# Optimization experiments

Measured on AMD Instinct MI355X. Metric: run time of the kernel, lower is better.

## Reference

```python
import jax, jax.numpy as jnp
import numpy as np

B, N, C, H = 2, 2048, 1024, 16
D = C // H  # head dim = 64
SCALE = 1.0 / np.sqrt(D)
BASE = 10000.0  # ntk_factor=1.0 => base unchanged


def setup_inputs() -> dict:
    key = jax.random.key(0)
    k1, k2, k3, k4 = jax.random.split(key, 4)
    x = jax.random.normal(k1, (B, N, C), dtype=jnp.float32)
    Wqkv = jax.random.normal(k2, (C, 3 * C), dtype=jnp.float32) * (1.0 / np.sqrt(C))
    Wout = jax.random.normal(k3, (C, C), dtype=jnp.float32) * (1.0 / np.sqrt(C))
    bout = jax.random.normal(k4, (C,), dtype=jnp.float32) * 0.01
    return {"x": x, "Wqkv": Wqkv, "Wout": Wout, "bout": bout}


def _rope_tables(n, d, dtype):
    inv_freq = 1.0 / (BASE ** (jnp.arange(0, d, 2, dtype=jnp.float32) / d))
    t = jnp.arange(n, dtype=jnp.float32)
    freqs = t[:, None] * inv_freq[None, :]            # [N, D/2]
    cos = jnp.cos(freqs)[None, :, None, :].astype(dtype)  # [1,N,1,D/2]
    sin = jnp.sin(freqs)[None, :, None, :].astype(dtype)
    return cos, sin


def _apply_rope(u, cos, sin):
    # u: [B,N,H,D]; strided-halves RoPE variant (cat, not interleave)
    u1, u2 = u[..., ::2], u[..., 1::2]
    return jnp.concatenate([u1 * cos - u2 * sin, u1 * sin + u2 * cos], axis=-1)


def reference(x, Wqkv, Wout, bout):
    b, n, c = x.shape
    qkv = (x @ Wqkv).reshape(b, n, 3, H, D)
    q, k, v = qkv[:, :, 0], qkv[:, :, 1], qkv[:, :, 2]  # [B,N,H,D]
    cos, sin = _rope_tables(n, D, x.dtype)
    q = _apply_rope(q, cos, sin)
    k = _apply_rope(k, cos, sin)
    scores = jnp.einsum("bqhd,bkhd->bhqk", q, k) * SCALE
    causal = jnp.triu(jnp.ones((n, n), dtype=bool), k=1)
    scores = jnp.where(causal, -jnp.inf, scores)
    attn = jax.nn.softmax(scores, axis=-1)
    out = jnp.einsum("bhqk,bkhd->bqhd", attn, v).reshape(b, n, c)
    return out @ Wout + bout
```

## Files before the change

### kernel.cpp

```cpp
#include <hip/hip_runtime.h>
#include <hip/hip_bf16.h>
#include <math.h>

#define B_ 2
#define N_ 2048
#define C_ 1024
#define H_ 16
#define D_ 64
#define M_ 4096
#define QKV_N 3072
#define SCALE_ 0.125f
#define FIXM 8.0f
#define L2E 1.442695041f

typedef unsigned short u16;
typedef unsigned int u32;
using bf16x8   = __attribute__((ext_vector_type(8))) __bf16;
using ushortx8 = __attribute__((ext_vector_type(8))) unsigned short;
using floatx4  = __attribute__((ext_vector_type(4))) float;

__device__ __forceinline__ float bf2f(u16 u) {
    union { u32 i; float f; } v; v.i = ((u32)u) << 16; return v.f;
}
__device__ __forceinline__ u16 f2bf(float f) {
    union { float f; u32 i; } v; v.f = f;
    u32 r = (v.i + 0x7fff + ((v.i >> 16) & 1)) >> 16;
    return (u16)r;
}
__device__ __forceinline__ u32 pk2bf(float a, float b) {
    __hip_bfloat162 h = __float22bfloat162_rn(make_float2(a, b));
    union { __hip_bfloat162 h; u32 u; } c; c.h = h; return c.u;
}

__device__ __forceinline__ void gl2lds16(const void* g, void* l) {
    __builtin_amdgcn_global_load_lds(
        (const __attribute__((address_space(1))) unsigned int*)(unsigned long long)g,
        (__attribute__((address_space(3))) unsigned int*)(unsigned long long)l,
        16, 0, 0);
}

__constant__ unsigned char UQI[24] = {7,15,15,14,14,6,13,13,12,12,5,11,11,10,10,4,9,9,8,8,3,2,1,0};
__constant__ unsigned char UT0[24] = {0,0,16,0,15,0,0,14,0,13,0,0,12,0,11,0,0,10,0,9,0,0,0,0};
__constant__ unsigned char UNT[24] = {16,16,16,15,15,14,14,14,13,13,12,12,12,11,11,10,10,10,9,9,8,6,4,2};

__device__ __forceinline__ void do_convtrans(const float* W, u16* Wt, int K, int N,
                                             int nb, int kb, int tid) {
    int n = nb * 256 + tid;
    int k0 = kb * 128;
    #pragma unroll
    for (int kk = 0; kk < 128; kk += 8) {
        ushortx8 v;
        #pragma unroll
        for (int j = 0; j < 8; j++)
            v[j] = f2bf(W[(size_t)(k0 + kk + j) * N + n]);
        *(ushortx8*)(&Wt[(size_t)n * K + k0 + kk]) = v;
    }
}

__global__ __launch_bounds__(256) void prep_kernel(
    const float* __restrict__ x, const float* __restrict__ Wqkv,
    float* __restrict__ cosT, float* __restrict__ sinT,
    u16* __restrict__ xb, u16* __restrict__ Wqkvt)
{
    int bid = blockIdx.x, tid = threadIdx.x;
    if (bid < 2048) {
        int i = bid * 256 + tid;
        const float4* p = (const float4*)x + (size_t)i * 2;
        float4 a = p[0], b = p[1];
        ushortx8 v;
        v[0] = f2bf(a.x); v[1] = f2bf(a.y); v[2] = f2bf(a.z); v[3] = f2bf(a.w);
        v[4] = f2bf(b.x); v[5] = f2bf(b.y); v[6] = f2bf(b.z); v[7] = f2bf(b.w);
        *(ushortx8*)(xb + (size_t)i * 8) = v;
    } else if (bid < 2304) {
        int idx = (bid - 2048) * 256 + tid;
        int n = idx >> 5, i = idx & 31;
        double inv = pow(10000.0, -(double)i / 32.0);
        double f = (double)n * inv;
        cosT[idx] = (float)cos(f);
        sinT[idx] = (float)sin(f);
    } else {
        int u = bid - 2304;
        do_convtrans(Wqkv, Wqkvt, C_, QKV_N, u % 12, u / 12, tid);
    }
}

__global__ __launch_bounds__(256) void gemm128(
    const u16* __restrict__ A, const u16* __restrict__ Bt,
    void* __restrict__ Cm, const float* __restrict__ bias, int fp32out,
    int M, int N, int K)
{
    __shared__ u16 As[128 * 32];
    __shared__ u16 Bs[128 * 32];
    const int t = threadIdx.x;
    const int w = t >> 6, lane = t & 63;
    const int quad = lane >> 4, cc = lane & 15;
    const int m0 = blockIdx.y * 128, n0 = blockIdx.x * 128;
    const int wm = (w >> 1) * 64, wn = (w & 1) * 64;

    floatx4 acc[4][4];
    floatx4 zero = {0.f, 0.f, 0.f, 0.f};
    #pragma unroll
    for (int i = 0; i < 4; i++)
        #pragma unroll
        for (int j = 0; j < 4; j++) acc[i][j] = zero;

    const int srow = lane >> 2, skof = (lane & 3) * 8;

    for (int k0 = 0; k0 < K; k0 += 32) {
        __syncthreads();
        #pragma unroll
        for (int c = 0; c < 2; c++) {
            int chunk = w * 2 + c;
            int row = chunk * 16 + srow;
            gl2lds16(A  + (size_t)(m0 + row) * K + k0 + skof, (char*)As + chunk * 1024);
            gl2lds16(Bt + (size_t)(n0 + row) * K + k0 + skof, (char*)Bs + chunk * 1024);
        }
        __syncthreads();

        bf16x8 af[4], bf[4];
        #pragma unroll
        for (int i = 0; i < 4; i++)
            af[i] = *(const bf16x8*)(&As[(wm + i * 16 + cc) * 32 + quad * 8]);
        #pragma unroll
        for (int j = 0; j < 4; j++)
            bf[j] = *(const bf16x8*)(&Bs[(wn + j * 16 + cc) * 32 + quad * 8]);
        #pragma unroll
        for (int i = 0; i < 4; i++)
            #pragma unroll
            for (int j = 0; j < 4; j++)
                acc[i][j] = __builtin_amdgcn_mfma_f32_16x16x32_bf16(af[i], bf[j], acc[i][j], 0, 0, 0);
    }

    #pragma unroll
    for (int i = 0; i < 4; i++)
        #pragma unroll
        for (int j = 0; j < 4; j++)
            #pragma unroll
            for (int r = 0; r < 4; r++) {
                int row = m0 + wm + i * 16 + quad * 4 + r;
                int col = n0 + wn + j * 16 + cc;
                float v = acc[i][j][r];
                if (fp32out) ((float*)Cm)[(size_t)row * N + col] = v + bias[col];
                else         ((u16*)Cm)[(size_t)row * N + col] = f2bf(v);
            }
}

__global__ void rope_kernel(const u16* __restrict__ qkv,
                            const float* __restrict__ cosT, const float* __restrict__ sinT,
                            u16* __restrict__ Qh, u16* __restrict__ Kh, u16* __restrict__ Vh)
{
    int idx = blockIdx.x * 256 + threadIdx.x;
    if (idx >= B_ * N_ * H_ * 32) return;
    int i = idx & 31;
    int h = (idx >> 5) & (H_ - 1);
    int n = (idx >> 9) & (N_ - 1);
    int b = idx >> 20;
    size_t m = (size_t)b * N_ + n;
    const u16* row = qkv + m * QKV_N;
    float cs = cosT[n * 32 + i], sn = sinT[n * 32 + i];

    float q1 = bf2f(row[h * 64 + 2 * i]),      q2 = bf2f(row[h * 64 + 2 * i + 1]);
    float k1 = bf2f(row[C_ + h * 64 + 2 * i]), k2 = bf2f(row[C_ + h * 64 + 2 * i + 1]);
    size_t obase = ((size_t)(b * H_ + h) * N_ + n) * D_;
    Qh[obase + i]      = f2bf((q1 * cs - q2 * sn) * SCALE_);
    Qh[obase + 32 + i] = f2bf((q1 * sn + q2 * cs) * SCALE_);
    Kh[obase + i]      = f2bf(k1 * cs - k2 * sn);
    Kh[obase + 32 + i] = f2bf(k1 * sn + k2 * cs);
    Vh[obase + 2 * i]     = row[2 * C_ + h * 64 + 2 * i];
    Vh[obase + 2 * i + 1] = row[2 * C_ + h * 64 + 2 * i + 1];
}

__global__ __launch_bounds__(256) void attn_kernel(
    const u16* __restrict__ Qh, const u16* __restrict__ Kh,
    const u16* __restrict__ Vh, u16* __restrict__ Ao,
    u16* __restrict__ Opart, float* __restrict__ lpart)
{
    constexpr int LDK = 66;
    __shared__ u16 Ks[2][64 * LDK];
    __shared__ u16 Vs[2][64 * LDK];
    __shared__ u16 Ps[4 * 32 * LDK];

    const int t = threadIdx.x;
    const int wave = t >> 6, lane = t & 63;
    const int quad = lane >> 4, cc = lane & 15;
    const int u = blockIdx.x;
    const int qi = UQI[u], tile0 = UT0[u], ntl = UNT[u];
    const int qb0 = qi * 128;
    const int bh = blockIdx.y;
    const size_t hb = (size_t)bh * N_ * D_;

    bf16x8 qf[2][2];
    #pragma unroll
    for (int qt = 0; qt < 2; qt++) {
        const u16* qrow = Qh + hb + (size_t)(qb0 + qt * 64 + wave * 16 + cc) * D_;
        qf[qt][0] = *(const bf16x8*)(qrow + quad * 8);
        qf[qt][1] = *(const bf16x8*)(qrow + 32 + quad * 8);
    }

    floatx4 zero = {0.f, 0.f, 0.f, 0.f};
    floatx4 Oacc[2][4];
    float lsum[2] = {0.f, 0.f};
    #pragma unroll
    for (int qt = 0; qt < 2; qt++)
        #pragma unroll
        for (int j = 0; j < 4; j++) Oacc[qt][j] = zero;

    const int krow = t >> 3, kch = (t & 7) * 8;
    const int kp = t >> 3, vchunk = (t & 7) * 8;
    const int qlocal = wave * 16 + cc;
    u32* psd = (u32*)Ps;

    bf16x8 kr[2]; ushortx8 vr[2];
    {
        int kb = tile0 * 64;
        kr[0] = *(const bf16x8*)(Kh + hb + (size_t)(kb + krow) * D_ + kch);
        kr[1] = *(const bf16x8*)(Kh + hb + (size_t)(kb + krow + 32) * D_ + kch);
        vr[0] = *(const ushortx8*)(Vh + hb + (size_t)(kb + 2 * kp) * D_ + vchunk);
        vr[1] = *(const ushortx8*)(Vh + hb + (size_t)(kb + 2 * kp + 1) * D_ + vchunk);
    }

    for (int ti = 0; ti < ntl; ti++) {
        const int kb = (tile0 + ti) * 64;
        const int c = ti & 1;
        *(bf16x8*)(&Ks[c][krow * LDK + kch]) = kr[0];
        *(bf16x8*)(&Ks[c][(krow + 32) * LDK + kch]) = kr[1];
        u32* vsd = (u32*)Vs[c];
        #pragma unroll
        for (int e = 0; e < 8; e++)
            vsd[(vchunk + e) * 33 + kp] = (u32)vr[0][e] | ((u32)vr[1][e] << 16);
        if (ti + 1 < ntl) {
            int kb2 = (tile0 + ti + 1) * 64;
            kr[0] = *(const bf16x8*)(Kh + hb + (size_t)(kb2 + krow) * D_ + kch);
            kr[1] = *(const bf16x8*)(Kh + hb + (size_t)(kb2 + krow + 32) * D_ + kch);
            vr[0] = *(const ushortx8*)(Vh + hb + (size_t)(kb2 + 2 * kp) * D_ + vchunk);
            vr[1] = *(const ushortx8*)(Vh + hb + (size_t)(kb2 + 2 * kp + 1) * D_ + vchunk);
        }
        __syncthreads();

        const bool act0 = (kb <= qb0);

        floatx4 S[2][4];
        #pragma unroll
        for (int nt = 0; nt < 4; nt++) {
            bf16x8 kf0 = *(const bf16x8*)(&Ks[c][(nt * 16 + cc) * LDK + quad * 8]);
            bf16x8 kf1 = *(const bf16x8*)(&Ks[c][(nt * 16 + cc) * LDK + 32 + quad * 8]);
            floatx4 a1 = zero;
            a1 = __builtin_amdgcn_mfma_f32_16x16x32_bf16(kf0, qf[1][0], a1, 0, 0, 0);
            a1 = __builtin_amdgcn_mfma_f32_16x16x32_bf16(kf1, qf[1][1], a1, 0, 0, 0);
            S[1][nt] = a1;
            if (act0) {
                floatx4 a0 = zero;
                a0 = __builtin_amdgcn_mfma_f32_16x16x32_bf16(kf0, qf[0][0], a0, 0, 0, 0);
                a0 = __builtin_amdgcn_mfma_f32_16x16x32_bf16(kf1, qf[0][1], a0, 0, 0, 0);
                S[0][nt] = a0;
            }
        }

        #pragma unroll
        for (int qt = 0; qt < 2; qt++) {
            if (qt == 0 && !act0) continue;
            const bool diag = (kb == qb0 + qt * 64);
            const int prow = (wave * 32 + qt * 16 + cc) * 33;
            #pragma unroll
            for (int nt = 0; nt < 4; nt++) {
                float p[4];
                #pragma unroll
                for (int r = 0; r < 4; r++) {
                    int key_l = nt * 16 + quad * 4 + r;
                    float e = exp2f(fmaf(S[qt][nt][r], L2E, -FIXM * L2E));
                    p[r] = (diag && (key_l > qlocal)) ? 0.0f : e;
                    lsum[qt] += p[r];
                }
                psd[prow + nt * 8 + quad * 2]     = pk2bf(p[0], p[1]);
                psd[prow + nt * 8 + quad * 2 + 1] = pk2bf(p[2], p[3]);
            }
        }

        #pragma unroll
        for (int s = 0; s < 2; s++) {
            bf16x8 pf1 = *(const bf16x8*)(&Ps[(wave * 32 + 16 + cc) * LDK + s * 32 + quad * 8]);
            bf16x8 pf0;
            if (act0) pf0 = *(const bf16x8*)(&Ps[(wave * 32 + cc) * LDK + s * 32 + quad * 8]);
            #pragma unroll
            for (int j = 0; j < 4; j++) {
                bf16x8 vf = *(const bf16x8*)(&Vs[c][(j * 16 + cc) * LDK + s * 32 + quad * 8]);
                Oacc[1][j] = __builtin_amdgcn_mfma_f32_16x16x32_bf16(pf1, vf, Oacc[1][j], 0, 0, 0);
                if (act0)
                    Oacc[0][j] = __builtin_amdgcn_mfma_f32_16x16x32_bf16(pf0, vf, Oacc[0][j], 0, 0, 0);
            }
        }
    }

    const bool partial = (qi >= 8);
    const int cid = (tile0 > 0) ? 1 : 0;
    const int slot = ((bh * 8 + (qi - 8)) * 2 + cid);
    const int b = bh >> 4, h = bh & (H_ - 1);

    #pragma unroll
    for (int qt = 0; qt < 2; qt++) {
        float lf = lsum[qt];
        lf += __shfl_xor(lf, 16, 64);
        lf += __shfl_xor(lf, 32, 64);
        if (!partial) {
            #pragma unroll
            for (int r = 0; r < 4; r++) {
                float l_r = __shfl(lf, quad * 4 + r, 64);
                float inv = 1.0f / l_r;
                int n = qb0 + qt * 64 + wave * 16 + quad * 4 + r;
                #pragma unroll
                for (int j = 0; j < 4; j++)
                    Ao[((size_t)b * N_ + n) * C_ + h * D_ + j * 16 + cc] = f2bf(Oacc[qt][j][r] * inv);
            }
        } else {
            #pragma unroll
            for (int r = 0; r < 4; r++) {
                int lrow = qt * 64 + wave * 16 + quad * 4 + r;
                u16* Ob = Opart + (size_t)slot * (128 * 64) + (size_t)lrow * 64;
                #pragma unroll
                for (int j = 0; j < 4; j++)
                    Ob[j * 16 + cc] = f2bf(Oacc[qt][j][r]);
            }
            if (lane < 16)
                lpart[slot * 128 + qt * 64 + wave * 16 + cc] = lf;
        }
    }
}

__global__ __launch_bounds__(256) void attn_combine(
    const u16* __restrict__ Opart, const float* __restrict__ lpart,
    u16* __restrict__ Ao, const float* __restrict__ Wout, u16* __restrict__ Woutt)
{
    if (blockIdx.x >= 2048) {
        int u = blockIdx.x - 2048;
        do_convtrans(Wout, Woutt, C_, C_, u % 4, u / 4, threadIdx.x);
        return;
    }
    int g = blockIdx.x * 256 + threadIdx.x;
    int f4 = g & 15;
    int row = (g >> 4) & 127;
    int qz = (g >> 11) & 7;
    int bh = g >> 14;
    int s0 = (bh * 8 + qz) * 2;
    const u16* O0 = Opart + (size_t)s0 * (128 * 64) + (size_t)row * 64 + f4 * 4;
    const u16* O1 = O0 + 128 * 64;
    float l = lpart[s0 * 128 + row] + lpart[(s0 + 1) * 128 + row];
    float inv = 1.0f / l;
    ushort4 a = *(const ushort4*)O0, c = *(const ushort4*)O1;
    int b = bh >> 4, h = bh & (H_ - 1);
    int n = (qz + 8) * 128 + row;
    u16* d = Ao + ((size_t)b * N_ + n) * C_ + h * D_ + f4 * 4;
    d[0] = f2bf((bf2f(a.x) + bf2f(c.x)) * inv);
    d[1] = f2bf((bf2f(a.y) + bf2f(c.y)) * inv);
    d[2] = f2bf((bf2f(a.z) + bf2f(c.z)) * inv);
    d[3] = f2bf((bf2f(a.w) + bf2f(c.w)) * inv);
}

extern "C" void kernel_launch(void* const* d_in, const int* in_sizes, int n_in,
                              void* d_out, int out_size, void* d_ws, size_t ws_size,
                              hipStream_t stream)
{
    const float* x    = (const float*)d_in[0];
    const float* Wqkv = (const float*)d_in[1];
    const float* Wout = (const float*)d_in[2];
    const float* bout = (const float*)d_in[3];

    char* p = (char*)d_ws;
    u16* qkv = (u16*)p; p += (size_t)M_ * QKV_N * 2;
    u16* Qh  = (u16*)p; p += (size_t)B_ * H_ * N_ * D_ * 2;
    u16* Kh  = (u16*)p; p += (size_t)B_ * H_ * N_ * D_ * 2;
    u16* Vh  = (u16*)p; p += (size_t)B_ * H_ * N_ * D_ * 2;
    u16* Ao  = (u16*)p; p += (size_t)M_ * C_ * 2;
    float* cosT = (float*)p; p += (size_t)N_ * 32 * 4;
    float* sinT = (float*)p; p += (size_t)N_ * 32 * 4;

    u16* xb    = Ao;
    u16* Wqkvt = Qh;
    u16* Woutt = qkv;
    u16* Opart = (u16*)((char*)qkv + ((size_t)2 << 20));
    float* lpart = (float*)((char*)qkv + ((size_t)21 << 20));

    hipLaunchKernelGGL(prep_kernel, dim3(2400), dim3(256), 0, stream,
                       x, Wqkv, cosT, sinT, xb, Wqkvt);
    hipLaunchKernelGGL(gemm128, dim3(QKV_N / 128, M_ / 128), dim3(256), 0, stream,
                       xb, Wqkvt, qkv, (const float*)nullptr, 0, M_, QKV_N, C_);
    hipLaunchKernelGGL(rope_kernel, dim3((B_ * N_ * H_ * 32) / 256), dim3(256), 0, stream,
                       qkv, cosT, sinT, Qh, Kh, Vh);
    hipLaunchKernelGGL(attn_kernel, dim3(24, B_ * H_), dim3(256), 0, stream,
                       Qh, Kh, Vh, Ao, Opart, lpart);
    hipLaunchKernelGGL(attn_combine, dim3(2048 + 32), dim3(256), 0, stream,
                       Opart, lpart, Ao, Wout, Woutt);
    hipLaunchKernelGGL(gemm128, dim3(C_ / 128, M_ / 128), dim3(256), 0, stream,
                       Ao, Woutt, d_out, bout, 1, M_, C_, C_);
}
```

Measured before the change: 230.0 us.

## Write V pre-transposed from QKV GEMM and drop LDS staging in attention

The QKV GEMM epilogue now writes V directly in a key-interleaved transposed layout, so the rope kernel no longer copies V. The attention kernel drops all shared-memory staging of K, V and P. It loads K fragments and transposed V fragments straight from global memory into registers, and keeps P in registers as MFMA operands. It also adds s_setprio around the MFMA bursts and an occupancy hint in launch_bounds. This removes LDS traffic and __syncthreads per tile, at the cost of more global and L2 loads, higher register pressure, and scattered 2-byte stores in the GEMM epilogue.

After: 256.1 us. 11.3% more time.

```diff
diff --git a/kernel.cpp b/kernel.cpp
--- a/kernel.cpp
+++ b/kernel.cpp
@@ -18,6 +18,8 @@
 using bf16x8   = __attribute__((ext_vector_type(8))) __bf16;
 using ushortx8 = __attribute__((ext_vector_type(8))) unsigned short;
 using floatx4  = __attribute__((ext_vector_type(4))) float;
+using u32x2    = __attribute__((ext_vector_type(2))) u32;
+using u32x4    = __attribute__((ext_vector_type(4))) u32;
 
 __device__ __forceinline__ float bf2f(u16 u) {
     union { u32 i; float f; } v; v.i = ((u32)u) << 16; return v.f;
@@ -87,6 +89,7 @@
 __global__ __launch_bounds__(256) void gemm128(
     const u16* __restrict__ A, const u16* __restrict__ Bt,
     void* __restrict__ Cm, const float* __restrict__ bias, int fp32out,
+    u16* __restrict__ Vt,
     int M, int N, int K)
 {
     __shared__ u16 As[128 * 32];
@@ -131,6 +134,23 @@
                 acc[i][j] = __builtin_amdgcn_mfma_f32_16x16x32_bf16(af[i], bf[j], acc[i][j], 0, 0, 0);
     }
 
+    if (Vt && n0 >= 2048) {
+        #pragma unroll
+        for (int i = 0; i < 4; i++)
+            #pragma unroll
+            for (int j = 0; j < 4; j++)
+                #pragma unroll
+                for (int r = 0; r < 4; r++) {
+                    int row = m0 + wm + i * 16 + quad * 4 + r;
+                    int col2 = n0 + wn + j * 16 + cc - 2048;
+                    int h = col2 >> 6, d = col2 & 63;
+                    int b = row >> 11, n = row & 2047;
+                    Vt[(size_t)(b * H_ + h) * (N_ * D_) + (size_t)(n >> 2) * 256 + d * 4 + (n & 3)]
+                        = f2bf(acc[i][j][r]);
+                }
+        return;
+    }
+
     #pragma unroll
     for (int i = 0; i < 4; i++)
         #pragma unroll
@@ -147,7 +167,7 @@
 
 __global__ void rope_kernel(const u16* __restrict__ qkv,
                             const float* __restrict__ cosT, const float* __restrict__ sinT,
-                            u16* __restrict__ Qh, u16* __restrict__ Kh, u16* __restrict__ Vh)
+                            u16* __restrict__ Qh, u16* __restrict__ Kh)
 {
     int idx = blockIdx.x * 256 + threadIdx.x;
     if (idx >= B_ * N_ * H_ * 32) return;
@@ -166,20 +186,13 @@
     Qh[obase + 32 + i] = f2bf((q1 * sn + q2 * cs) * SCALE_);
     Kh[obase + i]      = f2bf(k1 * cs - k2 * sn);
     Kh[obase + 32 + i] = f2bf(k1 * sn + k2 * cs);
-    Vh[obase + 2 * i]     = row[2 * C_ + h * 64 + 2 * i];
-    Vh[obase + 2 * i + 1] = row[2 * C_ + h * 64 + 2 * i + 1];
-}
-
-__global__ __launch_bounds__(256) void attn_kernel(
+}
+
+__global__ __launch_bounds__(256, 3) void attn_kernel(
     const u16* __restrict__ Qh, const u16* __restrict__ Kh,
-    const u16* __restrict__ Vh, u16* __restrict__ Ao,
+    const u16* __restrict__ Vt, u16* __restrict__ Ao,
     u16* __restrict__ Opart, float* __restrict__ lpart)
 {
-    constexpr int LDK = 66;
-    __shared__ u16 Ks[2][64 * LDK];
-    __shared__ u16 Vs[2][64 * LDK];
-    __shared__ u16 Ps[4 * 32 * LDK];
-
     const int t = threadIdx.x;
     const int wave = t >> 6, lane = t & 63;
     const int quad = lane >> 4, cc = lane & 15;
@@ -188,6 +201,7 @@
     const int qb0 = qi * 128;
     const int bh = blockIdx.y;
     const size_t hb = (size_t)bh * N_ * D_;
+    const int qlocal = wave * 16 + cc;
 
     bf16x8 qf[2][2];
     #pragma unroll
@@ -197,6 +211,9 @@
         qf[qt][1] = *(const bf16x8*)(qrow + 32 + quad * 8);
     }
 
+    const u16* Kb = Kh + hb + (size_t)cc * D_ + quad * 8;
+    const u16* Vb = Vt + hb + quad * 256 + cc * 4;
+
     floatx4 zero = {0.f, 0.f, 0.f, 0.f};
     floatx4 Oacc[2][4];
     float lsum[2] = {0.f, 0.f};
@@ -205,90 +222,118 @@
         #pragma unroll
         for (int j = 0; j < 4; j++) Oacc[qt][j] = zero;
 
-    const int krow = t >> 3, kch = (t & 7) * 8;
-    const int kp = t >> 3, vchunk = (t & 7) * 8;
-    const int qlocal = wave * 16 + cc;
-    u32* psd = (u32*)Ps;
-
-    bf16x8 kr[2]; ushortx8 vr[2];
+    bf16x8 kf[4][2];
     {
-        int kb = tile0 * 64;
-        kr[0] = *(const bf16x8*)(Kh + hb + (size_t)(kb + krow) * D_ + kch);
-        kr[1] = *(const bf16x8*)(Kh + hb + (size_t)(kb + krow + 32) * D_ + kch);
-        vr[0] = *(const ushortx8*)(Vh + hb + (size_t)(kb + 2 * kp) * D_ + vchunk);
-        vr[1] = *(const ushortx8*)(Vh + hb + (size_t)(kb + 2 * kp + 1) * D_ + vchunk);
+        const u16* kp = Kb + (size_t)(tile0 * 64) * D_;
+        #pragma unroll
+        for (int nt = 0; nt < 4; nt++) {
+            kf[nt][0] = *(const bf16x8*)(kp + nt * 16 * D_);
+            kf[nt][1] = *(const bf16x8*)(kp + nt * 16 * D_ + 32);
+        }
     }
 
     for (int ti = 0; ti < ntl; ti++) {
         const int kb = (tile0 + ti) * 64;
-        const int c = ti & 1;
-        *(bf16x8*)(&Ks[c][krow * LDK + kch]) = kr[0];
-        *(bf16x8*)(&Ks[c][(krow + 32) * LDK + kch]) = kr[1];
-        u32* vsd = (u32*)Vs[c];
-        #pragma unroll
-        for (int e = 0; e < 8; e++)
-            vsd[(vchunk + e) * 33 + kp] = (u32)vr[0][e] | ((u32)vr[1][e] << 16);
-        if (ti + 1 < ntl) {
-            int kb2 = (tile0 + ti + 1) * 64;
-            kr[0] = *(const bf16x8*)(Kh + hb + (size_t)(kb2 + krow) * D_ + kch);
-            kr[1] = *(const bf16x8*)(Kh + hb + (size_t)(kb2 + krow + 32) * D_ + kch);
-            vr[0] = *(const ushortx8*)(Vh + hb + (size_t)(kb2 + 2 * kp) * D_ + vchunk);
-            vr[1] = *(const ushortx8*)(Vh + hb + (size_t)(kb2 + 2 * kp + 1) * D_ + vchunk);
-        }
-        __syncthreads();
-
         const bool act0 = (kb <= qb0);
 
-        floatx4 S[2][4];
-        #pragma unroll
-        for (int nt = 0; nt < 4; nt++) {
-            bf16x8 kf0 = *(const bf16x8*)(&Ks[c][(nt * 16 + cc) * LDK + quad * 8]);
-            bf16x8 kf1 = *(const bf16x8*)(&Ks[c][(nt * 16 + cc) * LDK + 32 + quad * 8]);
-            floatx4 a1 = zero;
-            a1 = __builtin_amdgcn_mfma_f32_16x16x32_bf16(kf0, qf[1][0], a1, 0, 0, 0);
-            a1 = __builtin_amdgcn_mfma_f32_16x16x32_bf16(kf1, qf[1][1], a1, 0, 0, 0);
-            S[1][nt] = a1;
-            if (act0) {
-                floatx4 a0 = zero;
-                a0 = __builtin_amdgcn_mfma_f32_16x16x32_bf16(kf0, qf[0][0], a0, 0, 0, 0);
-                a0 = __builtin_amdgcn_mfma_f32_16x16x32_bf16(kf1, qf[0][1], a0, 0, 0, 0);
-                S[0][nt] = a0;
-            }
-        }
-
-        #pragma unroll
-        for (int qt = 0; qt < 2; qt++) {
-            if (qt == 0 && !act0) continue;
-            const bool diag = (kb == qb0 + qt * 64);
-            const int prow = (wave * 32 + qt * 16 + cc) * 33;
+        u32x2 vf[4][4];
+        {
+            const u16* vp = Vb + (size_t)kb * 64;
+            #pragma unroll
+            for (int nt = 0; nt < 4; nt++)
+                #pragma unroll
+                for (int j = 0; j < 4; j++)
+                    vf[nt][j] = *(const u32x2*)(vp + nt * 1024 + j * 64);
+        }
+
+        u32 pa[2][4][2];
+
+        {
+            floatx4 S[4];
+            __builtin_amdgcn_s_setprio(1);
+            #pragma unroll
+            for (int nt = 0; nt < 4; nt++) {
+                floatx4 a = zero;
+                a = __builtin_amdgcn_mfma_f32_16x16x32_bf16(kf[nt][0], qf[1][0], a, 0, 0, 0);
+                a = __builtin_amdgcn_mfma_f32_16x16x32_bf16(kf[nt][1], qf[1][1], a, 0, 0, 0);
+                S[nt] = a;
+            }
+            __builtin_amdgcn_s_setprio(0);
+            const bool diag = (kb == qb0 + 64);
             #pragma unroll
             for (int nt = 0; nt < 4; nt++) {
                 float p[4];
                 #pragma unroll
                 for (int r = 0; r < 4; r++) {
                     int key_l = nt * 16 + quad * 4 + r;
-                    float e = exp2f(fmaf(S[qt][nt][r], L2E, -FIXM * L2E));
+                    float e = exp2f(fmaf(S[nt][r], L2E, -FIXM * L2E));
                     p[r] = (diag && (key_l > qlocal)) ? 0.0f : e;
-                    lsum[qt] += p[r];
+                    lsum[1] += p[r];
                 }
-                psd[prow + nt * 8 + quad * 2]     = pk2bf(p[0], p[1]);
-                psd[prow + nt * 8 + quad * 2 + 1] = pk2bf(p[2], p[3]);
-            }
-        }
-
-        #pragma unroll
-        for (int s = 0; s < 2; s++) {
-            bf16x8 pf1 = *(const bf16x8*)(&Ps[(wave * 32 + 16 + cc) * LDK + s * 32 + quad * 8]);
-            bf16x8 pf0;
-            if (act0) pf0 = *(const bf16x8*)(&Ps[(wave * 32 + cc) * LDK + s * 32 + quad * 8]);
+                pa[1][nt][0] = pk2bf(p[0], p[1]);
+                pa[1][nt][1] = pk2bf(p[2], p[3]);
+            }
+        }
+
+        floatx4 S0[4];
+        if (act0) {
+            __builtin_amdgcn_s_setprio(1);
+            #pragma unroll
+            for (int nt = 0; nt < 4; nt++) {
+                floatx4 a = zero;
+                a = __builtin_amdgcn_mfma_f32_16x16x32_bf16(kf[nt][0], qf[0][0], a, 0, 0, 0);
+                a = __builtin_amdgcn_mfma_f32_16x16x32_bf16(kf[nt][1], qf[0][1], a, 0, 0, 0);
+                S0[nt] = a;
+            }
+            __builtin_amdgcn_s_setprio(0);
+        }
+
+        if (ti + 1 < ntl) {
+            const u16* kp = Kb + (size_t)(kb + 64) * D_;
+            #pragma unroll
+            for (int nt = 0; nt < 4; nt++) {
+                kf[nt][0] = *(const bf16x8*)(kp + nt * 16 * D_);
+                kf[nt][1] = *(const bf16x8*)(kp + nt * 16 * D_ + 32);
+            }
+        }
+
+        if (act0) {
+            const bool diag = (kb == qb0);
+            #pragma unroll
+            for (int nt = 0; nt < 4; nt++) {
+                float p[4];
+                #pragma unroll
+                for (int r = 0; r < 4; r++) {
+                    int key_l = nt * 16 + quad * 4 + r;
+                    float e = exp2f(fmaf(S0[nt][r], L2E, -FIXM * L2E));
+                    p[r] = (diag && (key_l > qlocal)) ? 0.0f : e;
+                    lsum[0] += p[r];
+                }
+                pa[0][nt][0] = pk2bf(p[0], p[1]);
+                pa[0][nt][1] = pk2bf(p[2], p[3]);
+            }
+        }
+
+        __builtin_amdgcn_s_setprio(1);
+        #pragma unroll
+        for (int g = 0; g < 2; g++) {
+            u32x4 aa1 = {pa[1][2 * g][0], pa[1][2 * g][1], pa[1][2 * g + 1][0], pa[1][2 * g + 1][1]};
+            bf16x8 A1 = __builtin_bit_cast(bf16x8, aa1);
+            bf16x8 A0;
+            if (act0) {
+                u32x4 aa0 = {pa[0][2 * g][0], pa[0][2 * g][1], pa[0][2 * g + 1][0], pa[0][2 * g + 1][1]};
+                A0 = __builtin_bit_cast(bf16x8, aa0);
+            }
             #pragma unroll
             for (int j = 0; j < 4; j++) {
-                bf16x8 vf = *(const bf16x8*)(&Vs[c][(j * 16 + cc) * LDK + s * 32 + quad * 8]);
-                Oacc[1][j] = __builtin_amdgcn_mfma_f32_16x16x32_bf16(pf1, vf, Oacc[1][j], 0, 0, 0);
+                u32x4 vv = {vf[2 * g][j][0], vf[2 * g][j][1], vf[2 * g + 1][j][0], vf[2 * g + 1][j][1]};
+                bf16x8 v8 = __builtin_bit_cast(bf16x8, vv);
+                Oacc[1][j] = __builtin_amdgcn_mfma_f32_16x16x32_bf16(A1, v8, Oacc[1][j], 0, 0, 0);
                 if (act0)
-                    Oacc[0][j] = __builtin_amdgcn_mfma_f32_16x16x32_bf16(pf0, vf, Oacc[0][j], 0, 0, 0);
-            }
-        }
+                    Oacc[0][j] = __builtin_amdgcn_mfma_f32_16x16x32_bf16(A0, v8, Oacc[0][j], 0, 0, 0);
+            }
+        }
+        __builtin_amdgcn_s_setprio(0);
     }
 
     const bool partial = (qi >= 8);
@@ -368,7 +413,7 @@
     u16* qkv = (u16*)p; p += (size_t)M_ * QKV_N * 2;
     u16* Qh  = (u16*)p; p += (size_t)B_ * H_ * N_ * D_ * 2;
     u16* Kh  = (u16*)p; p += (size_t)B_ * H_ * N_ * D_ * 2;
-    u16* Vh  = (u16*)p; p += (size_t)B_ * H_ * N_ * D_ * 2;
+    u16* Vt  = (u16*)p; p += (size_t)B_ * H_ * N_ * D_ * 2;
     u16* Ao  = (u16*)p; p += (size_t)M_ * C_ * 2;
     float* cosT = (float*)p; p += (size_t)N_ * 32 * 4;
     float* sinT = (float*)p; p += (size_t)N_ * 32 * 4;
@@ -382,13 +427,13 @@
     hipLaunchKernelGGL(prep_kernel, dim3(2400), dim3(256), 0, stream,
                        x, Wqkv, cosT, sinT, xb, Wqkvt);
     hipLaunchKernelGGL(gemm128, dim3(QKV_N / 128, M_ / 128), dim3(256), 0, stream,
-                       xb, Wqkvt, qkv, (const float*)nullptr, 0, M_, QKV_N, C_);
+                       xb, Wqkvt, qkv, (const float*)nullptr, 0, Vt, M_, QKV_N, C_);
     hipLaunchKernelGGL(rope_kernel, dim3((B_ * N_ * H_ * 32) / 256), dim3(256), 0, stream,
-                       qkv, cosT, sinT, Qh, Kh, Vh);
+                       qkv, cosT, sinT, Qh, Kh);
     hipLaunchKernelGGL(attn_kernel, dim3(24, B_ * H_), dim3(256), 0, stream,
-                       Qh, Kh, Vh, Ao, Opart, lpart);
+                       Qh, Kh, Vt, Ao, Opart, lpart);
     hipLaunchKernelGGL(attn_combine, dim3(2048 + 32), dim3(256), 0, stream,
                        Opart, lpart, Ao, Wout, Woutt);
     hipLaunchKernelGGL(gemm128, dim3(C_ / 128, M_ / 128), dim3(256), 0, stream,
-                       Ao, Woutt, d_out, bout, 1, M_, C_, C_);
-}
+                       Ao, Woutt, d_out, bout, 1, (u16*)nullptr, M_, C_, C_);
+}
```
